# Optimization experiments

Measured on AMD Instinct MI355X. Metric: run time of the kernel, lower is better.

The kernel has to match this reference:

```python
import jax, jax.numpy as jnp
import numpy as np

IN_CAPS, OUT_CAPS, OUT_DIM = 32, 10, 16


def squash(s):
    # s: [B, out_caps, out_dim]
    sq = jnp.sum(s * s, axis=2)              # [B, out_caps]
    mod = jnp.sqrt(sq)
    scale = sq / (1.0 + sq) / mod            # matches torch: sqrmod/(1+sqrmod)/mod
    return scale[..., None] * s


def setup_inputs() -> dict:
    key = jax.random.key(0)
    k1, k2 = jax.random.split(key)
    B, in_dim = 4096, 288
    caps_output = jax.random.normal(k1, (B, IN_CAPS, in_dim), dtype=jnp.float32)
    # W initialized uniform(-1/32, 1/32) in the original; scale randn similarly small
    W = jax.random.uniform(k2, (IN_CAPS, in_dim, OUT_CAPS * OUT_DIM),
                           dtype=jnp.float32, minval=-1.0 / 32, maxval=1.0 / 32)
    b = jnp.zeros((IN_CAPS, OUT_CAPS), dtype=jnp.float32)
    return {"caps_output": caps_output, "W": W, "b": b}


def reference(caps_output, W, b):
    B = caps_output.shape[0]
    # caps_output.unsqueeze(2).matmul(W): per-input-capsule matmul
    u = jnp.einsum('bni,nio->bno', caps_output, W)          # [B, 32, 160]
    u = u.reshape(B, IN_CAPS, OUT_CAPS, OUT_DIM)            # [B, 32, 10, 16]

    c = jax.nn.softmax(b, axis=1)                           # [32, 10]
    s = jnp.einsum('no,bnod->bod', c, u)                    # [B, 10, 16]
    v = squash(s)

    b_batch = jnp.broadcast_to(b, (B, IN_CAPS, OUT_CAPS))
    for _ in range(3):
        # agreement: <u_predict, v>
        b_batch = b_batch + jnp.einsum('bnod,bod->bno', u, v)
        c = jax.nn.softmax(b_batch, axis=-1)                # [B, 32, 10]
        s = jnp.einsum('bno,bnod->bod', c, u)
        v = squash(s)
    return v
```

## Files before the change

### kernel.cpp

```cpp
#include <hip/hip_runtime.h>
#include <hip/hip_bf16.h>

#define IN_CAPS 32
#define OUT_CAPS 10
#define NOUT 160
#define KDIM 288
#define BATCH 4096
#define KSTEPS 9
#define CTILES 10
#define STR2 162

typedef __bf16 bf16x8 __attribute__((ext_vector_type(8)));
typedef float  f32x4  __attribute__((ext_vector_type(4)));
typedef __attribute__((address_space(1))) void as1_t;
typedef __attribute__((address_space(3))) void as3_t;

__global__ __launch_bounds__(256) void prep_w(const float* __restrict__ W,
                                              __bf16* __restrict__ Wf) {
    int f = blockIdx.x * 256 + threadIdx.x;
    int j    = f & 7;
    int l    = (f >> 3) & 63;
    int rest = f >> 9;
    int c    = rest % CTILES;
    int tnk  = rest / CTILES;
    int ks   = tnk % KSTEPS;
    int n    = tnk / KSTEPS;
    int k    = ks * 32 + (l >> 4) * 8 + j;
    int col  = c * 16 + (l & 15);
    Wf[f] = (__bf16)W[(n * KDIM + k) * NOUT + col];
}

__device__ __forceinline__ void waitv(int n) {
    switch (n) {
        case 0:  asm volatile("s_waitcnt vmcnt(0)"  ::: "memory"); break;
        case 4:  asm volatile("s_waitcnt vmcnt(4)"  ::: "memory"); break;
        case 5:  asm volatile("s_waitcnt vmcnt(5)"  ::: "memory"); break;
        case 8:  asm volatile("s_waitcnt vmcnt(8)"  ::: "memory"); break;
        default: asm volatile("s_waitcnt vmcnt(10)" ::: "memory"); break;
    }
}

__global__ __launch_bounds__(256) void gemm_u(const float* __restrict__ caps,
                                              const __bf16* __restrict__ Wf,
                                              uint4* __restrict__ up) {
    __shared__ float  As[4][64 * 32];
    __shared__ __bf16 Bs[4][5120];

    const int lin  = blockIdx.x;
    const int n    = lin & 31;
    const int rb   = lin >> 5;
    const int w    = threadIdx.x >> 6;
    const int lane = threadIdx.x & 63;
    const int lm   = lane & 15;
    const int lk   = lane >> 4;

    const int sl0 = w * 128 + lane;
    const int sl1 = sl0 + 64;
    const int r0 = sl0 >> 3, r1 = sl1 >> 3;
    const int c0 = (sl0 & 7) ^ (r0 & 7);
    const int c1 = (sl1 & 7) ^ (r1 & 7);
    const float* ga0 = caps + ((size_t)(rb * 64 + r0) * IN_CAPS + n) * KDIM + c0 * 4;
    const float* ga1 = caps + ((size_t)(rb * 64 + r1) * IN_CAPS + n) * KDIM + c1 * 4;
    const __bf16* wb = Wf + (size_t)n * (KSTEPS * 5120);

#define STAGE(ks) do {                                                               \
    const int _bf = (ks) & 3;                                                        \
    __builtin_amdgcn_global_load_lds((const as1_t*)(ga0 + (ks) * 32),                \
                                     (as3_t*)&As[_bf][w * 512],        16, 0, 0);    \
    __builtin_amdgcn_global_load_lds((const as1_t*)(ga1 + (ks) * 32),                \
                                     (as3_t*)&As[_bf][w * 512 + 256],  16, 0, 0);    \
    __builtin_amdgcn_global_load_lds((const as1_t*)(wb + (size_t)(ks) * 5120 +       \
                                     (w * 2) * 512 + lane * 8),                      \
                                     (as3_t*)&Bs[_bf][(w * 2) * 512],  16, 0, 0);    \
    __builtin_amdgcn_global_load_lds((const as1_t*)(wb + (size_t)(ks) * 5120 +       \
                                     (w * 2 + 1) * 512 + lane * 8),                  \
                                     (as3_t*)&Bs[_bf][(w * 2 + 1) * 512], 16, 0, 0); \
    if (w < 2)                                                                       \
        __builtin_amdgcn_global_load_lds((const as1_t*)(wb + (size_t)(ks) * 5120 +   \
                                         (8 + w) * 512 + lane * 8),                  \
                                         (as3_t*)&Bs[_bf][(8 + w) * 512], 16, 0, 0); \
} while (0)

    f32x4 acc[CTILES];
#pragma unroll
    for (int ct = 0; ct < CTILES; ++ct) acc[ct] = (f32x4){0.f, 0.f, 0.f, 0.f};

    const int rl = w * 16 + lm;
    const int h0 = ((2 * lk)     ^ (lm & 7)) * 4;
    const int h1 = ((2 * lk + 1) ^ (lm & 7)) * 4;
    const int per_stage = (w < 2) ? 5 : 4;

    STAGE(0); STAGE(1); STAGE(2);

#pragma unroll
    for (int ks = 0; ks < KSTEPS; ++ks) {
        const int rem = (8 - ks) < 2 ? (8 - ks) : 2;
        waitv(per_stage * rem);
        __builtin_amdgcn_s_barrier();
        asm volatile("" ::: "memory");
        if (ks + 3 < KSTEPS) STAGE(ks + 3);

        const float*  Ac = As[ks & 3];
        const __bf16* Bc = Bs[ks & 3];
        f32x4 x0 = *(const f32x4*)&Ac[rl * 32 + h0];
        f32x4 x1 = *(const f32x4*)&Ac[rl * 32 + h1];
        bf16x8 a;
        a[0] = (__bf16)x0[0]; a[1] = (__bf16)x0[1];
        a[2] = (__bf16)x0[2]; a[3] = (__bf16)x0[3];
        a[4] = (__bf16)x1[0]; a[5] = (__bf16)x1[1];
        a[6] = (__bf16)x1[2]; a[7] = (__bf16)x1[3];

#pragma unroll
        for (int ct = 0; ct < CTILES; ++ct) {
            bf16x8 bfr = *(const bf16x8*)&Bc[ct * 512 + lane * 8];
            acc[ct] = __builtin_amdgcn_mfma_f32_16x16x32_bf16(a, bfr, acc[ct], 0, 0, 0);
        }
    }

    const int rw = rb * 2 + (w >> 1);
    const int mt = w & 1;
    const size_t cbase = ((((size_t)n * 128 + rw) * 2 + mt) * 5) * 64 + lane;
#pragma unroll
    for (int p = 0; p < 5; ++p) {
        bf16x8 pk;
#pragma unroll
        for (int j = 0; j < 8; ++j)
            pk[j] = (__bf16)acc[2 * p + (j >> 2)][j & 3];
        up[cbase + (size_t)p * 64] = __builtin_bit_cast(uint4, pk);
    }
#undef STAGE
}

__global__ __launch_bounds__(256) void routing(const uint4* __restrict__ up,
                                               const float* __restrict__ bbias,
                                               float* __restrict__ out) {
    __shared__ __bf16 ul[4][IN_CAPS * STR2];
    __shared__ float  bl[4][IN_CAPS * OUT_CAPS];
    __shared__ float  cs[4][IN_CAPS * OUT_CAPS];
    __shared__ float  ss[4][NOUT];
    __shared__ float  vs[4][NOUT];
    __shared__ float  scale_s[4][16];

    const int t  = threadIdx.x;
    const int b0 = blockIdx.x * 4;
    const int rw = b0 >> 5;
    const int mt = (b0 >> 4) & 1;
    const int lk = (b0 >> 2) & 3;

    for (int c = t; c < 2560; c += 256) {
        int n   = c / 80;
        int rem = c - n * 80;
        int p   = rem >> 4;
        int lm  = rem & 15;
        size_t idx = ((((size_t)n * 128 + rw) * 2 + mt) * 5 + p) * 64 + lk * 16 + lm;
        bf16x8 v = __builtin_bit_cast(bf16x8, up[idx]);
#pragma unroll
        for (int j = 0; j < 8; ++j) {
            int ct = 2 * p + (j >> 2);
            int rr = j & 3;
            ul[rr][n * STR2 + ct * 16 + lm] = v[j];
        }
    }
    const int grp = t >> 6;
    const int g   = t & 63;
    for (int pp = g; pp < IN_CAPS * OUT_CAPS; pp += 64) bl[grp][pp] = bbias[pp];
    __syncthreads();

    for (int it = 0; it < 4; ++it) {
        if (it > 0) {
            for (int pp = g; pp < IN_CAPS * OUT_CAPS; pp += 64) {
                int n = pp & 31;
                int o = pp >> 5;
                float a = 0.f;
#pragma unroll
                for (int d = 0; d < 16; ++d)
                    a += (float)ul[grp][n * STR2 + o * 16 + d] * vs[grp][o * 16 + d];
                bl[grp][n * 10 + o] += a;
            }
            __syncthreads();
        }
        if (g < IN_CAPS) {
            float m = bl[grp][g * 10];
#pragma unroll
            for (int o = 1; o < 10; ++o) m = fmaxf(m, bl[grp][g * 10 + o]);
            float e[10];
            float sum = 0.f;
#pragma unroll
            for (int o = 0; o < 10; ++o) { e[o] = __expf(bl[grp][g * 10 + o] - m); sum += e[o]; }
            float inv = 1.0f / sum;
#pragma unroll
            for (int o = 0; o < 10; ++o) cs[grp][g * 10 + o] = e[o] * inv;
        }
        __syncthreads();
        for (int p = g; p < NOUT; p += 64) {
            int o = p >> 4;
            float a = 0.f;
#pragma unroll
            for (int nn = 0; nn < IN_CAPS; ++nn)
                a += cs[grp][nn * 10 + o] * (float)ul[grp][nn * STR2 + p];
            ss[grp][p] = a;
        }
        __syncthreads();
        if (g < OUT_CAPS) {
            float sq = 0.f;
#pragma unroll
            for (int d = 0; d < 16; ++d) { float x = ss[grp][g * 16 + d]; sq += x * x; }
            scale_s[grp][g] = sq / ((1.0f + sq) * sqrtf(sq));
        }
        __syncthreads();
        for (int p = g; p < NOUT; p += 64) vs[grp][p] = scale_s[grp][p >> 4] * ss[grp][p];
        __syncthreads();
    }

    for (int p = g; p < NOUT; p += 64)
        out[(size_t)(b0 + grp) * NOUT + p] = vs[grp][p];
}

extern "C" void kernel_launch(void* const* d_in, const int* in_sizes, int n_in,
                              void* d_out, int out_size, void* d_ws, size_t ws_size,
                              hipStream_t stream) {
    const float* caps  = (const float*)d_in[0];
    const float* W     = (const float*)d_in[1];
    const float* bbias = (const float*)d_in[2];
    float* out = (float*)d_out;

    __bf16* Wf = (__bf16*)d_ws;
    uint4*  up = (uint4*)((char*)d_ws + 2949120);

    prep_w<<<dim3(5760), dim3(256), 0, stream>>>(W, Wf);
    gemm_u<<<dim3(2048), dim3(256), 0, stream>>>(caps, Wf, up);
    routing<<<dim3(BATCH / 4), dim3(256), 0, stream>>>(up, bbias, out);
}
```

Measured before the change: 83.64 us.

## Keep per-capsule W resident in LDS and stream A per wave without barriers

The GEMM kernel now loads the whole bf16 W slice for one input capsule (all 9 k-steps) into shared memory once per block. Each of 8 waves then independently streams four 16-row A tiles through a private 4-slot ring, using only vmcnt waits and no block barriers. The grid shrinks from 2048 blocks of 256 threads to 256 blocks of 512 threads, so W is fetched from global memory far fewer times. In exchange there is a large LDS footprint (about 92KB for W plus 64KB for A), which limits occupancy, a serial W load before compute starts, and only 256 blocks to fill the GPU.

```diff
diff --git a/kernel.cpp b/kernel.cpp
--- a/kernel.cpp
+++ b/kernel.cpp
@@ -33,100 +33,100 @@
 __device__ __forceinline__ void waitv(int n) {
     switch (n) {
         case 0:  asm volatile("s_waitcnt vmcnt(0)"  ::: "memory"); break;
+        case 2:  asm volatile("s_waitcnt vmcnt(2)"  ::: "memory"); break;
         case 4:  asm volatile("s_waitcnt vmcnt(4)"  ::: "memory"); break;
-        case 5:  asm volatile("s_waitcnt vmcnt(5)"  ::: "memory"); break;
-        case 8:  asm volatile("s_waitcnt vmcnt(8)"  ::: "memory"); break;
-        default: asm volatile("s_waitcnt vmcnt(10)" ::: "memory"); break;
-    }
-}
-
-__global__ __launch_bounds__(256) void gemm_u(const float* __restrict__ caps,
+        case 6:  asm volatile("s_waitcnt vmcnt(6)"  ::: "memory"); break;
+        case 9:  asm volatile("s_waitcnt vmcnt(9)"  ::: "memory"); break;
+        default: asm volatile("s_waitcnt vmcnt(11)" ::: "memory"); break;
+    }
+}
+
+__global__ __launch_bounds__(512) void gemm_u(const float* __restrict__ caps,
                                               const __bf16* __restrict__ Wf,
                                               uint4* __restrict__ up) {
-    __shared__ float  As[4][64 * 32];
-    __shared__ __bf16 Bs[4][5120];
+    __shared__ float  As[8][4][512];
+    __shared__ __bf16 Bs[KSTEPS * 5120];
 
     const int lin  = blockIdx.x;
     const int n    = lin & 31;
-    const int rb   = lin >> 5;
+    const int rg   = lin >> 5;
     const int w    = threadIdx.x >> 6;
     const int lane = threadIdx.x & 63;
     const int lm   = lane & 15;
     const int lk   = lane >> 4;
 
-    const int sl0 = w * 128 + lane;
-    const int sl1 = sl0 + 64;
-    const int r0 = sl0 >> 3, r1 = sl1 >> 3;
-    const int c0 = (sl0 & 7) ^ (r0 & 7);
-    const int c1 = (sl1 & 7) ^ (r1 & 7);
-    const float* ga0 = caps + ((size_t)(rb * 64 + r0) * IN_CAPS + n) * KDIM + c0 * 4;
-    const float* ga1 = caps + ((size_t)(rb * 64 + r1) * IN_CAPS + n) * KDIM + c1 * 4;
-    const __bf16* wb = Wf + (size_t)n * (KSTEPS * 5120);
-
-#define STAGE(ks) do {                                                               \
-    const int _bf = (ks) & 3;                                                        \
-    __builtin_amdgcn_global_load_lds((const as1_t*)(ga0 + (ks) * 32),                \
-                                     (as3_t*)&As[_bf][w * 512],        16, 0, 0);    \
-    __builtin_amdgcn_global_load_lds((const as1_t*)(ga1 + (ks) * 32),                \
-                                     (as3_t*)&As[_bf][w * 512 + 256],  16, 0, 0);    \
-    __builtin_amdgcn_global_load_lds((const as1_t*)(wb + (size_t)(ks) * 5120 +       \
-                                     (w * 2) * 512 + lane * 8),                      \
-                                     (as3_t*)&Bs[_bf][(w * 2) * 512],  16, 0, 0);    \
-    __builtin_amdgcn_global_load_lds((const as1_t*)(wb + (size_t)(ks) * 5120 +       \
-                                     (w * 2 + 1) * 512 + lane * 8),                  \
-                                     (as3_t*)&Bs[_bf][(w * 2 + 1) * 512], 16, 0, 0); \
-    if (w < 2)                                                                       \
-        __builtin_amdgcn_global_load_lds((const as1_t*)(wb + (size_t)(ks) * 5120 +   \
-                                         (8 + w) * 512 + lane * 8),                  \
-                                         (as3_t*)&Bs[_bf][(8 + w) * 512], 16, 0, 0); \
+    const int r0  = lane >> 3;
+    const int cc0 = (lane & 7) ^ (r0 & 7);
+    const int row0 = rg * 512 + w * 64;
+    const float* g0 = caps + ((size_t)(row0 + r0)     * IN_CAPS + n) * KDIM + cc0 * 4;
+    const float* g1 = caps + ((size_t)(row0 + 8 + r0) * IN_CAPS + n) * KDIM + cc0 * 4;
+
+#define STAGE(s_) do {                                                            \
+    const int c_ = (s_) / 9, k_ = (s_) % 9, sl_ = (s_) & 3;                       \
+    const size_t off_ = (size_t)c_ * 16 * IN_CAPS * KDIM + k_ * 32;               \
+    __builtin_amdgcn_global_load_lds((const as1_t*)(g0 + off_),                   \
+                                     (as3_t*)&As[w][sl_][0],   16, 0, 0);         \
+    __builtin_amdgcn_global_load_lds((const as1_t*)(g1 + off_),                   \
+                                     (as3_t*)&As[w][sl_][256], 16, 0, 0);         \
 } while (0)
 
+    STAGE(0); STAGE(1); STAGE(2);
+
+    const uint4* wsrc = (const uint4*)(Wf + (size_t)n * (KSTEPS * 5120));
+    uint4* bdst = (uint4*)Bs;
+    for (int i = threadIdx.x; i < KSTEPS * 5120 / 8; i += 512) bdst[i] = wsrc[i];
+    __syncthreads();
+
     f32x4 acc[CTILES];
 #pragma unroll
     for (int ct = 0; ct < CTILES; ++ct) acc[ct] = (f32x4){0.f, 0.f, 0.f, 0.f};
 
-    const int rl = w * 16 + lm;
     const int h0 = ((2 * lk)     ^ (lm & 7)) * 4;
     const int h1 = ((2 * lk + 1) ^ (lm & 7)) * 4;
-    const int per_stage = (w < 2) ? 5 : 4;
-
-    STAGE(0); STAGE(1); STAGE(2);
-
-#pragma unroll
-    for (int ks = 0; ks < KSTEPS; ++ks) {
-        const int rem = (8 - ks) < 2 ? (8 - ks) : 2;
-        waitv(per_stage * rem);
-        __builtin_amdgcn_s_barrier();
-        asm volatile("" ::: "memory");
-        if (ks + 3 < KSTEPS) STAGE(ks + 3);
-
-        const float*  Ac = As[ks & 3];
-        const __bf16* Bc = Bs[ks & 3];
-        f32x4 x0 = *(const f32x4*)&Ac[rl * 32 + h0];
-        f32x4 x1 = *(const f32x4*)&Ac[rl * 32 + h1];
+
+#pragma unroll
+    for (int s = 0; s < 36; ++s) {
+        const int c_ = s / 9, k_ = s % 9;
+        if (s + 3 < 36) STAGE(s + 3);
+
+        int wn;
+        if      (s >= 33)               wn = 2 * (35 - s);
+        else if (c_ > 0 && k_ == 0)     wn = 11;
+        else if (c_ > 0 && k_ <= 2)     wn = 9;
+        else                            wn = 6;
+        waitv(wn);
+
+        const float* Ac = &As[w][s & 3][0];
+        f32x4 x0 = *(const f32x4*)&Ac[lm * 32 + h0];
+        f32x4 x1 = *(const f32x4*)&Ac[lm * 32 + h1];
         bf16x8 a;
         a[0] = (__bf16)x0[0]; a[1] = (__bf16)x0[1];
         a[2] = (__bf16)x0[2]; a[3] = (__bf16)x0[3];
         a[4] = (__bf16)x1[0]; a[5] = (__bf16)x1[1];
         a[6] = (__bf16)x1[2]; a[7] = (__bf16)x1[3];
 
+        const __bf16* Bc = &Bs[k_ * 5120 + lane * 8];
 #pragma unroll
         for (int ct = 0; ct < CTILES; ++ct) {
-            bf16x8 bfr = *(const bf16x8*)&Bc[ct * 512 + lane * 8];
+            bf16x8 bfr = *(const bf16x8*)(Bc + ct * 512);
             acc[ct] = __builtin_amdgcn_mfma_f32_16x16x32_bf16(a, bfr, acc[ct], 0, 0, 0);
         }
-    }
-
-    const int rw = rb * 2 + (w >> 1);
-    const int mt = w & 1;
-    const size_t cbase = ((((size_t)n * 128 + rw) * 2 + mt) * 5) * 64 + lane;
-#pragma unroll
-    for (int p = 0; p < 5; ++p) {
-        bf16x8 pk;
-#pragma unroll
-        for (int j = 0; j < 8; ++j)
-            pk[j] = (__bf16)acc[2 * p + (j >> 2)][j & 3];
-        up[cbase + (size_t)p * 64] = __builtin_bit_cast(uint4, pk);
+
+        if (k_ == 8) {
+            const int rw = rg * 16 + w * 2 + (c_ >> 1);
+            const int mt = c_ & 1;
+            const size_t cbase = ((((size_t)n * 128 + rw) * 2 + mt) * 5) * 64 + lane;
+#pragma unroll
+            for (int p = 0; p < 5; ++p) {
+                bf16x8 pk;
+#pragma unroll
+                for (int j = 0; j < 8; ++j)
+                    pk[j] = (__bf16)acc[2 * p + (j >> 2)][j & 3];
+                up[cbase + (size_t)p * 64] = __builtin_bit_cast(uint4, pk);
+            }
+#pragma unroll
+            for (int ct = 0; ct < CTILES; ++ct) acc[ct] = (f32x4){0.f, 0.f, 0.f, 0.f};
+        }
     }
 #undef STAGE
 }
@@ -228,6 +228,6 @@
     uint4*  up = (uint4*)((char*)d_ws + 2949120);
 
     prep_w<<<dim3(5760), dim3(256), 0, stream>>>(W, Wf);
-    gemm_u<<<dim3(2048), dim3(256), 0, stream>>>(caps, Wf, up);
+    gemm_u<<<dim3(256), dim3(512), 0, stream>>>(caps, Wf, up);
     routing<<<dim3(BATCH / 4), dim3(256), 0, stream>>>(up, bbias, out);
 }
```

Result: faster. 79.76 us (-4.6%).
